# Kernel optimization log

Hardware: AMD Instinct MI355X
Metric: run time of the kernel (lower is better)

## Reference

```python
import jax, jax.numpy as jnp
import numpy as np

BETA = 0.95      # LIF membrane decay (init arg)
THR = 1.0        # snntorch Leaky default threshold
NUM_STEPS = 128


@jax.custom_vjp
def spike(x):
    # Heaviside fire with ATan surrogate gradient (snntorch default, alpha=2)
    return (x > 0).astype(x.dtype)

def _spike_fwd(x):
    return spike(x), x

def _spike_bwd(x, g):
    return (g / (1.0 + (jnp.pi * x) ** 2),)

spike.defvjp(_spike_fwd, _spike_bwd)


def setup_inputs() -> dict:
    key = jax.random.key(0)
    ks = jax.random.split(key, 5)
    B, NI, NH, NO = 2048, 1024, 2048, 10
    return {
        "x": jax.random.normal(ks[0], (B, NI), dtype=jnp.float32),
        "w1": jax.random.normal(ks[1], (NH, NI), dtype=jnp.float32) * 0.05,
        "b1": jax.random.normal(ks[2], (NH,), dtype=jnp.float32) * 0.05,
        "w2": jax.random.normal(ks[3], (NO, NH), dtype=jnp.float32) * 0.05,
        "b2": jax.random.normal(ks[4], (NO,), dtype=jnp.float32) * 0.05,
    }


def reference(x, w1, b1, w2, b2):
    # fc1(x) is loop-invariant: compute the input current once.
    cur1 = jnp.einsum("bi,hi->bh", x, w1) + b1  # [B, NH]
    mem1_0 = jnp.zeros_like(cur1)
    mem2_0 = jnp.zeros((x.shape[0], w2.shape[0]), dtype=x.dtype)

    def step(carry, _):
        mem1, mem2 = carry
        # snntorch Leaky, reset-by-subtraction; reset term is detached.
        reset1 = jax.lax.stop_gradient((mem1 > THR).astype(mem1.dtype))
        mem1 = BETA * mem1 + cur1 - reset1 * THR
        spk1 = spike(mem1 - THR)
        cur2 = jnp.einsum("bh,oh->bo", spk1, w2) + b2  # [B, NO]
        reset2 = jax.lax.stop_gradient((mem2 > THR).astype(mem2.dtype))
        mem2 = BETA * mem2 + cur2 - reset2 * THR
        spk2 = spike(mem2 - THR)
        return (mem1, mem2), (spk2, mem2)

    _, (spk2_rec, mem2_rec) = jax.lax.scan(step, (mem1_0, mem2_0), None, length=NUM_STEPS)
    return spk2_rec, mem2_rec  # each [T, B, NO]
```

## Files before the change

### kernel.cpp

```cpp
#include <hip/hip_runtime.h>
#include <hip/hip_bf16.h>


#define B_   2048
#define NI_  1024
#define NH_  2048
#define NO_  10
#define T_   128
#define GB_  8
#define NBLK (B_ / GB_)
#define TC_  16
#define NCH  (T_ / TC_)

typedef __attribute__((ext_vector_type(8))) short short8;
typedef __attribute__((ext_vector_type(4))) float f32x4;
typedef __attribute__((ext_vector_type(4))) unsigned int u32x4;

__device__ __forceinline__ unsigned int bf16_rne(float f) {
  unsigned int u = __float_as_uint(f);
  return (u + 0x7FFFu + ((u >> 16) & 1u)) >> 16;
}

#define G_ASTRIDE 144
#define G_AOFF    0
#define G_BOFF    (128 * G_ASTRIDE)
#define G_SMEM    (2 * 128 * G_ASTRIDE)

__global__ __launch_bounds__(512, 2) void gemm_cur1(
    const float* __restrict__ x, const float* __restrict__ w1,
    const float* __restrict__ b1, float* __restrict__ cur1) {
  __shared__ __align__(16) char smem[G_SMEM];
  const int tid = threadIdx.x;
  const int lane = tid & 63;
  const int wv = tid >> 6;
  const int wm = wv >> 2;
  const int wn = wv & 3;
  const int n15 = lane & 15;
  const int g = lane >> 4;
  const int brow = blockIdx.y * 128;
  const int bcol = blockIdx.x * 128;

  const int r_st = tid >> 3;
  const int kq = tid & 7;

  f32x4 acc[4][2];
#pragma unroll
  for (int tm = 0; tm < 4; ++tm)
#pragma unroll
    for (int tn = 0; tn < 2; ++tn) acc[tm][tn] = f32x4{0, 0, 0, 0};

  for (int kt = 0; kt < NI_; kt += 32) {
#pragma unroll
    for (int p = 0; p < 2; ++p) {
      const int r = r_st + p * 64;
      const float4 va = *reinterpret_cast<const float4*>(
          &x[(size_t)(brow + r) * NI_ + kt + kq * 4]);
      const float4 vb = *reinterpret_cast<const float4*>(
          &w1[(size_t)(bcol + r) * NI_ + kt + kq * 4]);
      const float fa[4] = {va.x, va.y, va.z, va.w};
      const float fb[4] = {vb.x, vb.y, vb.z, vb.w};
      unsigned ha[4], la[4], hb[4], lb[4];
#pragma unroll
      for (int c = 0; c < 4; ++c) {
        ha[c] = bf16_rne(fa[c]);
        la[c] = bf16_rne(fa[c] - __uint_as_float(ha[c] << 16));
        hb[c] = bf16_rne(fb[c]);
        lb[c] = bf16_rne(fb[c] - __uint_as_float(hb[c] << 16));
      }
      char* arow = smem + G_AOFF + r * G_ASTRIDE;
      char* brw  = smem + G_BOFF + r * G_ASTRIDE;
      *reinterpret_cast<uint2*>(arow + kq * 8) =
          uint2{ha[0] | (ha[1] << 16), ha[2] | (ha[3] << 16)};
      *reinterpret_cast<uint2*>(arow + 64 + kq * 8) =
          uint2{la[0] | (la[1] << 16), la[2] | (la[3] << 16)};
      *reinterpret_cast<uint2*>(brw + kq * 8) =
          uint2{hb[0] | (hb[1] << 16), hb[2] | (hb[3] << 16)};
      *reinterpret_cast<uint2*>(brw + 64 + kq * 8) =
          uint2{lb[0] | (lb[1] << 16), lb[2] | (lb[3] << 16)};
    }
    __syncthreads();

    short8 ah[4], al[4], bh2[2], bl2[2];
#pragma unroll
    for (int tm = 0; tm < 4; ++tm) {
      const char* p = smem + G_AOFF + (wm * 64 + tm * 16 + n15) * G_ASTRIDE;
      ah[tm] = *reinterpret_cast<const short8*>(p + g * 16);
      al[tm] = *reinterpret_cast<const short8*>(p + 64 + g * 16);
    }
#pragma unroll
    for (int tn = 0; tn < 2; ++tn) {
      const char* p = smem + G_BOFF + (wn * 32 + tn * 16 + n15) * G_ASTRIDE;
      bh2[tn] = *reinterpret_cast<const short8*>(p + g * 16);
      bl2[tn] = *reinterpret_cast<const short8*>(p + 64 + g * 16);
    }
#pragma unroll
    for (int tm = 0; tm < 4; ++tm)
#pragma unroll
      for (int tn = 0; tn < 2; ++tn) {
        acc[tm][tn] = __builtin_amdgcn_mfma_f32_16x16x32_bf16(
            ah[tm], bh2[tn], acc[tm][tn], 0, 0, 0);
        acc[tm][tn] = __builtin_amdgcn_mfma_f32_16x16x32_bf16(
            ah[tm], bl2[tn], acc[tm][tn], 0, 0, 0);
        acc[tm][tn] = __builtin_amdgcn_mfma_f32_16x16x32_bf16(
            al[tm], bh2[tn], acc[tm][tn], 0, 0, 0);
      }
    __syncthreads();
  }

#pragma unroll
  for (int tn = 0; tn < 2; ++tn) {
    const int col = bcol + wn * 32 + tn * 16 + n15;
    const float bias = b1[col];
#pragma unroll
    for (int tm = 0; tm < 4; ++tm) {
      const int rowb = brow + wm * 64 + tm * 16 + g * 4;
#pragma unroll
      for (int r = 0; r < 4; ++r)
        cur1[(size_t)(rowb + r) * NH_ + col] = acc[tm][tn][r] + bias;
    }
  }
}

#define LUT_OFF  0
#define BITS_OFF 128
#define BITS_PAR 8320
#define COMB_OFF 66688
#define COMB_PAR 10240
#define SMEM_BYTES 148608

__global__ __launch_bounds__(1024, 1) void snn_loop(
    const float* __restrict__ cur1, const float* __restrict__ w2,
    const float* __restrict__ b2, float* __restrict__ spk2_rec,
    float* __restrict__ mem2_rec) {
  extern __shared__ char smem[];
  uint2* lutw = reinterpret_cast<uint2*>(smem + LUT_OFF);
  const uint2* lut = lutw;
  float* comb = reinterpret_cast<float*>(smem + COMB_OFF);
  const int tid = threadIdx.x;
  const int lane = tid & 63;
  const int w = tid >> 6;
  const int bq = w & 7;
  const int hf = w >> 3;
  const int kc = w >> 1;
  const int bset = w & 1;
  const int bbase = blockIdx.x * GB_;

  if (tid < 16) {
    lutw[tid] = uint2{(tid & 1 ? 0x3F80u : 0u) | (tid & 2 ? 0x3F800000u : 0u),
                      (tid & 4 ? 0x3F80u : 0u) | (tid & 8 ? 0x3F800000u : 0u)};
  }

  float mem1[16], c1v[16], c1m[16], cc[16];
  {
    const float* base = cur1 + (size_t)(bbase + bq) * NH_ + hf * 1024 + lane * 16;
#pragma unroll
    for (int q = 0; q < 4; ++q) {
      const float4 v = *reinterpret_cast<const float4*>(base + q * 4);
      c1v[q * 4 + 0] = v.x; c1v[q * 4 + 1] = v.y;
      c1v[q * 4 + 2] = v.z; c1v[q * 4 + 3] = v.w;
    }
#pragma unroll
    for (int i = 0; i < 16; ++i) {
      mem1[i] = 0.0f;
      c1m[i] = c1v[i] - 1.0f;
      cc[i] = c1v[i];
    }
  }

  u32x4 bhi[8];
  {
    const int o = lane & 15;
    const int koff = (lane >> 4) * 8;
#pragma unroll
    for (int kbl = 0; kbl < 8; ++kbl) {
      const int kb = kc * 8 + kbl;
      unsigned int hw[4];
#pragma unroll
      for (int p = 0; p < 4; ++p) {
        unsigned int h0 = 0, h1 = 0;
        if (o < NO_) {
          const int k = kb * 32 + koff + p * 2;
          h0 = bf16_rne(w2[(size_t)o * NH_ + k]);
          h1 = bf16_rne(w2[(size_t)o * NH_ + k + 1]);
        }
        hw[p] = h0 | (h1 << 16);
      }
      bhi[kbl] = u32x4{hw[0], hw[1], hw[2], hw[3]};
    }
  }

  float mem2 = 0.0f, spk2 = 0.0f, b2v = 0.0f;
  float *srec = nullptr, *mrec = nullptr;
  if (w < 8 && lane < NO_) {
    b2v = b2[lane];
    srec = spk2_rec + (size_t)(bbase + w) * NO_ + lane;
    mrec = mem2_rec + (size_t)(bbase + w) * NO_ + lane;
  }

  const int n15 = lane & 15;
  const int g = lane >> 4;
  const unsigned char* bytes = reinterpret_cast<const unsigned char*>(smem);

  const int bits_hw = (hf * 32 + (lane >> 1)) * 2 + (lane & 1);

  auto P1_STEP = [&](unsigned short* bitsP16, int tl) {
    unsigned W = 0;
#pragma unroll
    for (int i = 15; i >= 0; --i) {
      const float m = fmaf(0.95f, mem1[i], cc[i]);
      mem1[i] = m;
      const bool c = m > 1.0f;
      W = W + W + (c ? 1u : 0u);
      cc[i] = c ? c1m[i] : c1v[i];
    }
    bitsP16[(bq * TC_ + tl) * 130 + bits_hw] = (unsigned short)W;
  };

  {
    unsigned short* b16 = reinterpret_cast<unsigned short*>(smem + BITS_OFF);
    for (int tl = 0; tl < TC_; ++tl) P1_STEP(b16, tl);
  }
  __syncthreads();

  for (int ch = 0; ch < NCH; ++ch) {
    const int cur = ch & 1;
    unsigned short* bitsN16 = reinterpret_cast<unsigned short*>(
        smem + BITS_OFF + (cur ^ 1) * (BITS_PAR * 4));
    float* combC = comb + cur * COMB_PAR;
    const float* combV = comb + (cur ^ 1) * COMB_PAR;
    const int bbyte = BITS_OFF + cur * (BITS_PAR * 4);

    if (ch > 0 && w < 8 && lane < NO_) {
      const float* cbase = combV + w * 160 + lane * 4;
#pragma unroll
      for (int tl = 0; tl < TC_; ++tl) {
        const int off = (tl >> 2) * 40 + (tl & 3);
        float s = 0.0f;
#pragma unroll
        for (int kk = 0; kk < 8; ++kk) s += cbase[kk * 1280 + off];
        const float cur2 = s + b2v;
        float m = fmaf(0.95f, mem2, cur2);
        m = m - spk2;
        mem2 = m;
        spk2 = (m > 1.0f) ? 1.0f : 0.0f;
        const int t = (ch - 1) * TC_ + tl;
        srec[(size_t)t * (B_ * NO_)] = spk2;
        mrec[(size_t)t * (B_ * NO_)] = m;
      }
    }

#pragma unroll
    for (int bi = 0; bi < 4; ++bi) {
      const int b = bset * 4 + bi;
      const int rbase = bbyte + ((b * TC_ + n15) * 65 + kc * 8) * 4 + g;
      f32x4 acc = {0.0f, 0.0f, 0.0f, 0.0f};
#pragma unroll
      for (int kbl = 0; kbl < 8; ++kbl) {
        const unsigned byt = bytes[rbase + kbl * 4];
        const uint2 lo2 = lut[byt & 15u];
        const uint2 hi2 = lut[byt >> 4];
        const u32x4 A = {lo2.x, lo2.y, hi2.x, hi2.y};
        const short8 af = __builtin_bit_cast(short8, A);
        acc = __builtin_amdgcn_mfma_f32_16x16x32_bf16(
            af, __builtin_bit_cast(short8, bhi[kbl]), acc, 0, 0, 0);
      }
      if (n15 < NO_)
        *reinterpret_cast<f32x4*>(
            &combC[((kc * 8 + b) * 4 + g) * 40 + n15 * 4]) = acc;
      if (ch < NCH - 1) {
        P1_STEP(bitsN16, 4 * bi);
        P1_STEP(bitsN16, 4 * bi + 1);
        P1_STEP(bitsN16, 4 * bi + 2);
        P1_STEP(bitsN16, 4 * bi + 3);
      }
    }

    __syncthreads();
  }

  if (w < 8 && lane < NO_) {
    const float* cbase = comb + ((NCH - 1) & 1) * COMB_PAR + w * 160 + lane * 4;
#pragma unroll
    for (int tl = 0; tl < TC_; ++tl) {
      const int off = (tl >> 2) * 40 + (tl & 3);
      float s = 0.0f;
#pragma unroll
      for (int kk = 0; kk < 8; ++kk) s += cbase[kk * 1280 + off];
      const float cur2 = s + b2v;
      float m = fmaf(0.95f, mem2, cur2);
      m = m - spk2;
      mem2 = m;
      spk2 = (m > 1.0f) ? 1.0f : 0.0f;
      const int t = (NCH - 1) * TC_ + tl;
      srec[(size_t)t * (B_ * NO_)] = spk2;
      mrec[(size_t)t * (B_ * NO_)] = m;
    }
  }
}

extern "C" void kernel_launch(void* const* d_in, const int* in_sizes, int n_in,
                              void* d_out, int out_size, void* d_ws, size_t ws_size,
                              hipStream_t stream) {
  const float* x  = (const float*)d_in[0];
  const float* w1 = (const float*)d_in[1];
  const float* b1 = (const float*)d_in[2];
  const float* w2 = (const float*)d_in[3];
  const float* b2 = (const float*)d_in[4];
  float* out = (float*)d_out;
  float* cur1 = (float*)d_ws;

  float* spk2_rec = out;
  float* mem2_rec = out + (size_t)T_ * B_ * NO_;

  (void)hipFuncSetAttribute(reinterpret_cast<const void*>(snn_loop),
                            hipFuncAttributeMaxDynamicSharedMemorySize,
                            SMEM_BYTES);

  dim3 g1(NH_ / 128, B_ / 128);
  gemm_cur1<<<g1, 512, 0, stream>>>(x, w1, b1, cur1);
  snn_loop<<<NBLK, 1024, SMEM_BYTES, stream>>>(cur1, w2, b2, spk2_rec, mem2_rec);
}
```

Baseline: 184.3 us.

## Split fused SNN loop into separate spike-generation and output-layer kernels

The single 1024-thread snn_loop kernel, which used 148 KB of dynamic shared memory and ran only 256 blocks, is replaced by two kernels. A spikegen kernel (1024 blocks) computes layer-1 membrane updates and writes packed spike bits to global workspace. An snn_out kernel (512 blocks) then stages those bits into shared memory, runs the bf16 MFMA layer-2 matvec and integrates mem2. The aim is higher occupancy and more parallelism across the GPU, at the cost of a global round trip for the spike bits (64 MB), an extra launch, and losing the old overlap between spike generation and MFMA. The GEMM loop also loads the A fragments per tm instead of all up front, which reduces register pressure.

```diff
diff --git a/kernel.cpp b/kernel.cpp
--- a/kernel.cpp
+++ b/kernel.cpp
@@ -7,10 +7,6 @@
 #define NH_  2048
 #define NO_  10
 #define T_   128
-#define GB_  8
-#define NBLK (B_ / GB_)
-#define TC_  16
-#define NCH  (T_ / TC_)
 
 typedef __attribute__((ext_vector_type(8))) short short8;
 typedef __attribute__((ext_vector_type(4))) float f32x4;
@@ -39,7 +35,6 @@
   const int g = lane >> 4;
   const int brow = blockIdx.y * 128;
   const int bcol = blockIdx.x * 128;
-
   const int r_st = tid >> 3;
   const int kq = tid & 7;
 
@@ -80,13 +75,7 @@
     }
     __syncthreads();
 
-    short8 ah[4], al[4], bh2[2], bl2[2];
-#pragma unroll
-    for (int tm = 0; tm < 4; ++tm) {
-      const char* p = smem + G_AOFF + (wm * 64 + tm * 16 + n15) * G_ASTRIDE;
-      ah[tm] = *reinterpret_cast<const short8*>(p + g * 16);
-      al[tm] = *reinterpret_cast<const short8*>(p + 64 + g * 16);
-    }
+    short8 bh2[2], bl2[2];
 #pragma unroll
     for (int tn = 0; tn < 2; ++tn) {
       const char* p = smem + G_BOFF + (wn * 32 + tn * 16 + n15) * G_ASTRIDE;
@@ -94,16 +83,20 @@
       bl2[tn] = *reinterpret_cast<const short8*>(p + 64 + g * 16);
     }
 #pragma unroll
-    for (int tm = 0; tm < 4; ++tm)
+    for (int tm = 0; tm < 4; ++tm) {
+      const char* p = smem + G_AOFF + (wm * 64 + tm * 16 + n15) * G_ASTRIDE;
+      const short8 ah = *reinterpret_cast<const short8*>(p + g * 16);
+      const short8 al = *reinterpret_cast<const short8*>(p + 64 + g * 16);
 #pragma unroll
       for (int tn = 0; tn < 2; ++tn) {
         acc[tm][tn] = __builtin_amdgcn_mfma_f32_16x16x32_bf16(
-            ah[tm], bh2[tn], acc[tm][tn], 0, 0, 0);
+            ah, bh2[tn], acc[tm][tn], 0, 0, 0);
         acc[tm][tn] = __builtin_amdgcn_mfma_f32_16x16x32_bf16(
-            ah[tm], bl2[tn], acc[tm][tn], 0, 0, 0);
+            ah, bl2[tn], acc[tm][tn], 0, 0, 0);
         acc[tm][tn] = __builtin_amdgcn_mfma_f32_16x16x32_bf16(
-            al[tm], bh2[tn], acc[tm][tn], 0, 0, 0);
-      }
+            al, bh2[tn], acc[tm][tn], 0, 0, 0);
+      }
+    }
     __syncthreads();
   }
 
@@ -121,50 +114,63 @@
   }
 }
 
-#define LUT_OFF  0
-#define BITS_OFF 128
-#define BITS_PAR 8320
-#define COMB_OFF 66688
-#define COMB_PAR 10240
-#define SMEM_BYTES 148608
-
-__global__ __launch_bounds__(1024, 1) void snn_loop(
-    const float* __restrict__ cur1, const float* __restrict__ w2,
+__global__ __launch_bounds__(512, 2) void spikegen(
+    const float* __restrict__ cur1, unsigned char* __restrict__ bits8) {
+  const int lane = threadIdx.x & 63;
+  const int w = threadIdx.x >> 6;
+  const int bq = w >> 2;
+  const int qf = w & 3;
+  const int bb = blockIdx.x * 2 + bq;
+
+  float mem1[8], c1v[8], c1m[8], cc[8];
+  {
+    const float* base = cur1 + (size_t)bb * NH_ + qf * 512 + lane * 8;
+#pragma unroll
+    for (int q = 0; q < 2; ++q) {
+      const float4 v = *reinterpret_cast<const float4*>(base + q * 4);
+      c1v[q * 4 + 0] = v.x; c1v[q * 4 + 1] = v.y;
+      c1v[q * 4 + 2] = v.z; c1v[q * 4 + 3] = v.w;
+    }
+#pragma unroll
+    for (int i = 0; i < 8; ++i) {
+      mem1[i] = 0.0f;
+      c1m[i] = c1v[i] - 1.0f;
+      cc[i] = c1v[i];
+    }
+  }
+
+  unsigned char* dst = bits8 + (size_t)bb * T_ * 256 + qf * 64 + lane;
+  for (int t = 0; t < T_; ++t) {
+    unsigned W = 0;
+#pragma unroll
+    for (int i = 7; i >= 0; --i) {
+      const float m = fmaf(0.95f, mem1[i], cc[i]);
+      mem1[i] = m;
+      const bool c = m > 1.0f;
+      W = W + W + (c ? 1u : 0u);
+      cc[i] = c ? c1m[i] : c1v[i];
+    }
+    dst[t * 256] = (unsigned char)W;
+  }
+}
+
+#define SO_TC 16
+
+__global__ __launch_bounds__(512, 2) void snn_out(
+    const unsigned* __restrict__ bitsg, const float* __restrict__ w2,
     const float* __restrict__ b2, float* __restrict__ spk2_rec,
     float* __restrict__ mem2_rec) {
-  extern __shared__ char smem[];
-  uint2* lutw = reinterpret_cast<uint2*>(smem + LUT_OFF);
-  const uint2* lut = lutw;
-  float* comb = reinterpret_cast<float*>(smem + COMB_OFF);
+  __shared__ uint2 lut[16];
+  __shared__ __align__(16) unsigned bitsl[64 * 68];
+  __shared__ __align__(16) float comb[8 * 640];
   const int tid = threadIdx.x;
   const int lane = tid & 63;
   const int w = tid >> 6;
-  const int bq = w & 7;
-  const int hf = w >> 3;
-  const int kc = w >> 1;
-  const int bset = w & 1;
-  const int bbase = blockIdx.x * GB_;
+  const int bbase = blockIdx.x * 4;
 
   if (tid < 16) {
-    lutw[tid] = uint2{(tid & 1 ? 0x3F80u : 0u) | (tid & 2 ? 0x3F800000u : 0u),
-                      (tid & 4 ? 0x3F80u : 0u) | (tid & 8 ? 0x3F800000u : 0u)};
-  }
-
-  float mem1[16], c1v[16], c1m[16], cc[16];
-  {
-    const float* base = cur1 + (size_t)(bbase + bq) * NH_ + hf * 1024 + lane * 16;
-#pragma unroll
-    for (int q = 0; q < 4; ++q) {
-      const float4 v = *reinterpret_cast<const float4*>(base + q * 4);
-      c1v[q * 4 + 0] = v.x; c1v[q * 4 + 1] = v.y;
-      c1v[q * 4 + 2] = v.z; c1v[q * 4 + 3] = v.w;
-    }
-#pragma unroll
-    for (int i = 0; i < 16; ++i) {
-      mem1[i] = 0.0f;
-      c1m[i] = c1v[i] - 1.0f;
-      cc[i] = c1v[i];
-    }
+    lut[tid] = uint2{(tid & 1 ? 0x3F80u : 0u) | (tid & 2 ? 0x3F800000u : 0u),
+                     (tid & 4 ? 0x3F80u : 0u) | (tid & 8 ? 0x3F800000u : 0u)};
   }
 
   u32x4 bhi[8];
@@ -173,7 +179,7 @@
     const int koff = (lane >> 4) * 8;
 #pragma unroll
     for (int kbl = 0; kbl < 8; ++kbl) {
-      const int kb = kc * 8 + kbl;
+      const int kb = w * 8 + kbl;
       unsigned int hw[4];
 #pragma unroll
       for (int p = 0; p < 4; ++p) {
@@ -191,7 +197,7 @@
 
   float mem2 = 0.0f, spk2 = 0.0f, b2v = 0.0f;
   float *srec = nullptr, *mrec = nullptr;
-  if (w < 8 && lane < NO_) {
+  if (w < 4 && lane < NO_) {
     b2v = b2[lane];
     srec = spk2_rec + (size_t)(bbase + w) * NO_ + lane;
     mrec = mem2_rec + (size_t)(bbase + w) * NO_ + lane;
@@ -199,60 +205,24 @@
 
   const int n15 = lane & 15;
   const int g = lane >> 4;
-  const unsigned char* bytes = reinterpret_cast<const unsigned char*>(smem);
-
-  const int bits_hw = (hf * 32 + (lane >> 1)) * 2 + (lane & 1);
-
-  auto P1_STEP = [&](unsigned short* bitsP16, int tl) {
-    unsigned W = 0;
-#pragma unroll
-    for (int i = 15; i >= 0; --i) {
-      const float m = fmaf(0.95f, mem1[i], cc[i]);
-      mem1[i] = m;
-      const bool c = m > 1.0f;
-      W = W + W + (c ? 1u : 0u);
-      cc[i] = c ? c1m[i] : c1v[i];
-    }
-    bitsP16[(bq * TC_ + tl) * 130 + bits_hw] = (unsigned short)W;
-  };
-
-  {
-    unsigned short* b16 = reinterpret_cast<unsigned short*>(smem + BITS_OFF);
-    for (int tl = 0; tl < TC_; ++tl) P1_STEP(b16, tl);
-  }
-  __syncthreads();
-
-  for (int ch = 0; ch < NCH; ++ch) {
-    const int cur = ch & 1;
-    unsigned short* bitsN16 = reinterpret_cast<unsigned short*>(
-        smem + BITS_OFF + (cur ^ 1) * (BITS_PAR * 4));
-    float* combC = comb + cur * COMB_PAR;
-    const float* combV = comb + (cur ^ 1) * COMB_PAR;
-    const int bbyte = BITS_OFF + cur * (BITS_PAR * 4);
-
-    if (ch > 0 && w < 8 && lane < NO_) {
-      const float* cbase = combV + w * 160 + lane * 4;
-#pragma unroll
-      for (int tl = 0; tl < TC_; ++tl) {
-        const int off = (tl >> 2) * 40 + (tl & 3);
-        float s = 0.0f;
-#pragma unroll
-        for (int kk = 0; kk < 8; ++kk) s += cbase[kk * 1280 + off];
-        const float cur2 = s + b2v;
-        float m = fmaf(0.95f, mem2, cur2);
-        m = m - spk2;
-        mem2 = m;
-        spk2 = (m > 1.0f) ? 1.0f : 0.0f;
-        const int t = (ch - 1) * TC_ + tl;
-        srec[(size_t)t * (B_ * NO_)] = spk2;
-        mrec[(size_t)t * (B_ * NO_)] = m;
-      }
-    }
-
-#pragma unroll
-    for (int bi = 0; bi < 4; ++bi) {
-      const int b = bset * 4 + bi;
-      const int rbase = bbyte + ((b * TC_ + n15) * 65 + kc * 8) * 4 + g;
+  const unsigned char* bytes = reinterpret_cast<const unsigned char*>(bitsl);
+
+  for (int ch = 0; ch < T_ / SO_TC; ++ch) {
+#pragma unroll
+    for (int j = 0; j < 2; ++j) {
+      const int q = tid + j * 512;
+      const int row = q >> 4;
+      const int kq = q & 15;
+      const int b = row >> 4, tl = row & 15;
+      const uint4 v = *reinterpret_cast<const uint4*>(
+          bitsg + ((size_t)(bbase + b) * T_ + ch * SO_TC + tl) * 64 + kq * 4);
+      *reinterpret_cast<uint4*>(bitsl + row * 68 + kq * 4) = v;
+    }
+    __syncthreads();
+
+#pragma unroll
+    for (int b = 0; b < 4; ++b) {
+      const int rbase = ((b * SO_TC + n15) * 68 + w * 8) * 4 + g;
       f32x4 acc = {0.0f, 0.0f, 0.0f, 0.0f};
 #pragma unroll
       for (int kbl = 0; kbl < 8; ++kbl) {
@@ -266,37 +236,33 @@
       }
       if (n15 < NO_)
         *reinterpret_cast<f32x4*>(
-            &combC[((kc * 8 + b) * 4 + g) * 40 + n15 * 4]) = acc;
-      if (ch < NCH - 1) {
-        P1_STEP(bitsN16, 4 * bi);
-        P1_STEP(bitsN16, 4 * bi + 1);
-        P1_STEP(bitsN16, 4 * bi + 2);
-        P1_STEP(bitsN16, 4 * bi + 3);
-      }
-    }
-
-    __syncthreads();
-  }
-
-  if (w < 8 && lane < NO_) {
-    const float* cbase = comb + ((NCH - 1) & 1) * COMB_PAR + w * 160 + lane * 4;
-#pragma unroll
-    for (int tl = 0; tl < TC_; ++tl) {
-      const int off = (tl >> 2) * 40 + (tl & 3);
-      float s = 0.0f;
-#pragma unroll
-      for (int kk = 0; kk < 8; ++kk) s += cbase[kk * 1280 + off];
-      const float cur2 = s + b2v;
-      float m = fmaf(0.95f, mem2, cur2);
-      m = m - spk2;
-      mem2 = m;
-      spk2 = (m > 1.0f) ? 1.0f : 0.0f;
-      const int t = (NCH - 1) * TC_ + tl;
-      srec[(size_t)t * (B_ * NO_)] = spk2;
-      mrec[(size_t)t * (B_ * NO_)] = m;
-    }
-  }
-}
+            &comb[w * 640 + b * 160 + g * 40 + n15 * 4]) = acc;
+    }
+    __syncthreads();
+
+    if (w < 4 && lane < NO_) {
+      const float* cbase = comb + w * 160 + lane * 4;
+#pragma unroll
+      for (int tl = 0; tl < SO_TC; ++tl) {
+        const int off = (tl >> 2) * 40 + (tl & 3);
+        float s = 0.0f;
+#pragma unroll
+        for (int kk = 0; kk < 8; ++kk) s += cbase[kk * 640 + off];
+        const float cur2 = s + b2v;
+        float m = fmaf(0.95f, mem2, cur2);
+        m = m - spk2;
+        mem2 = m;
+        spk2 = (m > 1.0f) ? 1.0f : 0.0f;
+        const int t = ch * SO_TC + tl;
+        srec[(size_t)t * (B_ * NO_)] = spk2;
+        mrec[(size_t)t * (B_ * NO_)] = m;
+      }
+    }
+  }
+}
+
+#define CUR1_BYTES ((size_t)B_ * NH_ * 4)
+#define BITS_BYTES ((size_t)B_ * T_ * 64 * 4)
 
 extern "C" void kernel_launch(void* const* d_in, const int* in_sizes, int n_in,
                               void* d_out, int out_size, void* d_ws, size_t ws_size,
@@ -308,15 +274,13 @@
   const float* b2 = (const float*)d_in[4];
   float* out = (float*)d_out;
   float* cur1 = (float*)d_ws;
+  unsigned* bitsg = (unsigned*)((char*)d_ws + CUR1_BYTES);
 
   float* spk2_rec = out;
   float* mem2_rec = out + (size_t)T_ * B_ * NO_;
 
-  (void)hipFuncSetAttribute(reinterpret_cast<const void*>(snn_loop),
-                            hipFuncAttributeMaxDynamicSharedMemorySize,
-                            SMEM_BYTES);
-
   dim3 g1(NH_ / 128, B_ / 128);
   gemm_cur1<<<g1, 512, 0, stream>>>(x, w1, b1, cur1);
-  snn_loop<<<NBLK, 1024, SMEM_BYTES, stream>>>(cur1, w2, b2, spk2_rec, mem2_rec);
-}
+  spikegen<<<B_ / 2, 512, 0, stream>>>(cur1, (unsigned char*)bitsg);
+  snn_out<<<B_ / 4, 512, 0, stream>>>(bitsg, w2, b2, spk2_rec, mem2_rec);
+}
```

New measurement: 174.1 us. -5.5%, faster.
